# Performance work log

Hardware: AMD Instinct MI355X
Metric: run time of the kernel (lower is better)

The kernel has to match this reference:

```python
import jax, jax.numpy as jnp
import numpy as np

B_, S, I, H = 16, 2048, 256, 512


def setup_inputs() -> dict:
    key = jax.random.key(0)
    k0, k1, k2, k3, k4 = jax.random.split(key, 5)
    x = jax.random.normal(k0, (B_, S, I), dtype=jnp.float32)
    # stable LRU parameterization: lambda = exp(-exp(nu) + i*theta), |lambda| < 1
    nu = jax.random.uniform(k1, (H,), dtype=jnp.float32, minval=-3.0, maxval=0.0)
    theta = jax.random.uniform(k2, (H,), dtype=jnp.float32, minval=0.0, maxval=2.0 * np.pi)
    scale = np.float32(1.0 / np.sqrt(2 * I))
    B_re = jax.random.normal(k3, (H, I), dtype=jnp.float32) * scale
    B_im = jax.random.normal(k4, (H, I), dtype=jnp.float32) * scale
    return {"x": x, "nu": nu, "theta": theta, "B_re": B_re, "B_im": B_im}


def reference(x, nu, theta, B_re, B_im):
    # complex diagonal recurrence matrix, shape [H]
    lam = jnp.exp(-jnp.exp(nu) + 1j * theta).astype(jnp.complex64)
    # complex input projection Bx_t = (B_re + i B_im) @ x_t, shape [batch, seq, H]
    Bx = (jnp.einsum('bsi,hi->bsh', x, B_re)
          + 1j * jnp.einsum('bsi,hi->bsh', x, B_im)).astype(jnp.complex64)
    Bx_t = jnp.swapaxes(Bx, 0, 1)  # [seq, batch, H] for scan over time
    h0 = jnp.zeros((x.shape[0], lam.shape[0]), dtype=jnp.complex64)

    def step(h, bx):
        h = lam * h + bx  # h_t = lambda * h_{t-1} + B x_t
        return h, h

    _, outs = jax.lax.scan(step, h0, Bx_t)  # [seq, batch, H] complex
    outs = jnp.swapaxes(outs, 0, 1)  # [batch, seq, H]
    # concat_real_imag: [batch, seq, 2H] float32
    return jnp.concatenate([outs.real, outs.imag], axis=-1)
```

## Files before the change

### kernel.cpp

```cpp
#include <hip/hip_runtime.h>
#include <cstdint>
#include <cstddef>

#define BB 16
#define SS 2048
#define II 256
#define HH 512
#define MM (BB * SS)
#define NNC 1024
#define CHUNK 64
#define NCHUNK (SS / CHUNK)

using bf16x8 = __attribute__((ext_vector_type(8))) short;
using short8 = __attribute__((ext_vector_type(8))) short;
using f32x4  = __attribute__((ext_vector_type(4))) float;

typedef __attribute__((address_space(3))) uint32_t       lds_u32;
typedef __attribute__((address_space(1))) const uint32_t glb_u32;

__device__ __forceinline__ short f2bf(float f) {
    uint32_t u = __float_as_uint(f);
    u += 0x7fffu + ((u >> 16) & 1u);
    return (short)(u >> 16);
}
__device__ __forceinline__ uint32_t packf16(float a, float b) {
    union { _Float16 h[2]; uint32_t u; } cv;
    cv.h[0] = (_Float16)a; cv.h[1] = (_Float16)b;
    return cv.u;
}
__device__ __forceinline__ float2 unpackf16(uint32_t u) {
    union { uint32_t u; _Float16 h[2]; } cv; cv.u = u;
    return make_float2((float)cv.h[0], (float)cv.h[1]);
}

__global__ __launch_bounds__(256) void cvt_xb(const float4* __restrict__ x,
                                              short8* __restrict__ xb,
                                              const float* __restrict__ Bre,
                                              const float* __restrict__ Bim,
                                              short* __restrict__ Bc) {
    const int bid = blockIdx.x;
    if (bid < 4096) {
        int i = bid * 256 + threadIdx.x;
        float4 v0 = x[2 * i], v1 = x[2 * i + 1];
        short8 o;
        o[0]=f2bf(v0.x); o[1]=f2bf(v0.y); o[2]=f2bf(v0.z); o[3]=f2bf(v0.w);
        o[4]=f2bf(v1.x); o[5]=f2bf(v1.y); o[6]=f2bf(v1.z); o[7]=f2bf(v1.w);
        xb[i] = o;
    } else {
        int idx = (bid - 4096) * 256 + threadIdx.x;
        int row = idx >> 5;
        int k0  = (idx & 31) << 3;
        const float* src = ((row & 1) ? Bim : Bre) + (size_t)(row >> 1) * II + k0;
        float4 v0 = *(const float4*)src;
        float4 v1 = *(const float4*)(src + 4);
        short8 o;
        o[0]=f2bf(v0.x); o[1]=f2bf(v0.y); o[2]=f2bf(v0.z); o[3]=f2bf(v0.w);
        o[4]=f2bf(v1.x); o[5]=f2bf(v1.y); o[6]=f2bf(v1.z); o[7]=f2bf(v1.w);
        *(short8*)(Bc + (size_t)row * II + k0) = o;
    }
}

__global__ __launch_bounds__(256, 3) void gemm_pack(const short* __restrict__ Xb,
                                                    const short* __restrict__ Bc,
                                                    uint32_t* __restrict__ Y) {
    __shared__ short Al[2][128 * 32];
    __shared__ short Bl[2][128 * 32];

    const int xcd = blockIdx.x & 7;
    const int k   = blockIdx.x >> 3;
    const int mt  = xcd * 32 + (k >> 3);
    const int nt  = k & 7;
    const int m0 = mt * 128, n0 = nt * 128;
    const int t  = threadIdx.x;
    const int w  = t >> 6, l = t & 63;
    const int fr = l & 15, fg = l >> 4;
    const int wr = w >> 1, wc = w & 1;

    f32x4 acc[4][4] = {};

#pragma unroll
    for (int i = 0; i < 2; ++i) {
        const int ch = i * 256 + t;
        __builtin_amdgcn_global_load_lds(
            (glb_u32*)(Xb + (size_t)(m0 + (ch >> 2)) * II + ((ch & 3) << 3)),
            (lds_u32*)&Al[0][ch * 8], 16, 0, 0);
        __builtin_amdgcn_global_load_lds(
            (glb_u32*)(Bc + (size_t)(n0 + (ch >> 2)) * II + ((ch & 3) << 3)),
            (lds_u32*)&Bl[0][ch * 8], 16, 0, 0);
    }
    __syncthreads();

    for (int ks = 0; ks < 8; ++ks) {
        const int cur = ks & 1, nxt = cur ^ 1;
        if (ks < 7) {
#pragma unroll
            for (int i = 0; i < 2; ++i) {
                const int ch = i * 256 + t;
                __builtin_amdgcn_global_load_lds(
                    (glb_u32*)(Xb + (size_t)(m0 + (ch >> 2)) * II + (ks + 1) * 32 + ((ch & 3) << 3)),
                    (lds_u32*)&Al[nxt][ch * 8], 16, 0, 0);
                __builtin_amdgcn_global_load_lds(
                    (glb_u32*)(Bc + (size_t)(n0 + (ch >> 2)) * II + (ks + 1) * 32 + ((ch & 3) << 3)),
                    (lds_u32*)&Bl[nxt][ch * 8], 16, 0, 0);
            }
        }
        bf16x8 a[4], b[4];
#pragma unroll
        for (int mi = 0; mi < 4; ++mi)
            a[mi] = *(const bf16x8*)&Al[cur][(wr * 64 + mi * 16 + fr) * 32 + fg * 8];
#pragma unroll
        for (int ni = 0; ni < 4; ++ni)
            b[ni] = *(const bf16x8*)&Bl[cur][(wc * 64 + ni * 16 + fr) * 32 + fg * 8];
#pragma unroll
        for (int mi = 0; mi < 4; ++mi)
#pragma unroll
            for (int ni = 0; ni < 4; ++ni)
                acc[mi][ni] = __builtin_amdgcn_mfma_f32_16x16x32_bf16(
                    a[mi], b[ni], acc[mi][ni], 0, 0, 0);
        __syncthreads();
    }

#pragma unroll
    for (int mi = 0; mi < 4; ++mi)
#pragma unroll
        for (int ni = 0; ni < 4; ++ni) {
            const int row0 = m0 + wr * 64 + mi * 16 + fg * 4;
            const int ncol = n0 + wc * 64 + ni * 16 + fr;
#pragma unroll
            for (int r = 0; r < 4; ++r) {
                float v = acc[mi][ni][r];
                float o = __shfl_xor(v, 1);
                if (!(fr & 1))
                    Y[(size_t)(row0 + r) * HH + (ncol >> 1)] = packf16(v, o);
            }
        }
}

__global__ __launch_bounds__(512) void scan_e(const uint32_t* __restrict__ Y,
                                              const float* __restrict__ nu,
                                              const float* __restrict__ th,
                                              float2* __restrict__ E) {
    const int g = blockIdx.x;
    const int b = g >> 5, c = g & 31;
    const int h = threadIdx.x;
    const float env = __expf(nu[h]);
    const float rad = __expf(-env);
    float s, cs; __sincosf(th[h], &s, &cs);
    const float lre = rad * cs, lim = rad * s;
    const uint32_t* base = Y + ((size_t)b * SS + (size_t)c * CHUNK) * HH + h;
    float hre = 0.f, him = 0.f;
#pragma unroll 8
    for (int t = 0; t < CHUNK; ++t) {
        float2 y = unpackf16(base[(size_t)t * HH]);
        const float nr = lre * hre - lim * him + y.x;
        him = lre * him + lim * hre + y.y;
        hre = nr;
    }
    E[(size_t)g * HH + h] = make_float2(hre, him);
}

__global__ __launch_bounds__(512) void scan_final(const uint32_t* __restrict__ Y,
                                                  const float2* __restrict__ E,
                                                  const float* __restrict__ nu,
                                                  const float* __restrict__ th,
                                                  float* __restrict__ out) {
    const int g = blockIdx.x;
    const int b = g >> 5, c = g & 31;
    const int h = threadIdx.x;
    const float env = __expf(nu[h]);
    const float rad = __expf(-env);
    float s, cs; __sincosf(th[h], &s, &cs);
    const float lre = rad * cs, lim = rad * s;

    const float rL = __expf(-(float)CHUNK * env);
    float sL, cL; __sincosf((float)CHUNK * th[h], &sL, &cL);
    const float l64re = rL * cL, l64im = rL * sL;
    float pre = 0.f, pim = 0.f;
    for (int j = 0; j < c; ++j) {
        const float2 e = E[((size_t)(b * NCHUNK + j)) * HH + h];
        const float nr = l64re * pre - l64im * pim + e.x;
        pim = l64re * pim + l64im * pre + e.y;
        pre = nr;
    }

    float hre = pre, him = pim;
    const uint32_t* yb = Y + ((size_t)b * SS + (size_t)c * CHUNK) * HH + h;
    float* ob = out + ((size_t)b * SS + (size_t)c * CHUNK) * NNC;
#pragma unroll 4
    for (int t = 0; t < CHUNK; ++t) {
        float2 y = unpackf16(yb[(size_t)t * HH]);
        const float nr = lre * hre - lim * him + y.x;
        him = lre * him + lim * hre + y.y;
        hre = nr;
        ob[(size_t)t * NNC + h]      = hre;
        ob[(size_t)t * NNC + HH + h] = him;
    }
}

extern "C" void kernel_launch(void* const* d_in, const int* in_sizes, int n_in,
                              void* d_out, int out_size, void* d_ws, size_t ws_size,
                              hipStream_t stream) {
    const float* x   = (const float*)d_in[0];
    const float* nu  = (const float*)d_in[1];
    const float* th  = (const float*)d_in[2];
    const float* Bre = (const float*)d_in[3];
    const float* Bim = (const float*)d_in[4];
    float* out = (float*)d_out;

    char* ws = (char*)d_ws;
    short*    Xb = (short*)ws;
    short*    Bc = (short*)(ws + (size_t)MM * II * 2);
    uint32_t* Y  = (uint32_t*)(ws + (size_t)MM * II * 2 + (size_t)NNC * II * 2);
    float2*   E  = (float2*)((char*)Y + (size_t)MM * HH * 4);

    cvt_xb<<<4096 + 128, 256, 0, stream>>>((const float4*)x, (short8*)Xb, Bre, Bim, Bc);
    gemm_pack<<<(MM / 128) * (NNC / 128), 256, 0, stream>>>(Xb, Bc, Y);
    scan_e<<<BB * NCHUNK, HH, 0, stream>>>(Y, nu, th, E);
    scan_final<<<BB * NCHUNK, HH, 0, stream>>>(Y, E, nu, th, out);
}
```

Measured before the change: 90.61 us.

## Fuse x fp32-to-bf16 conversion into GEMM A-tile loading

Removes the separate pass that converted x to bf16 in a workspace buffer. The GEMM now reads fp32 x directly into registers, converts it, and writes it to a padded LDS tile (row stride 40), with the next tile's loads issued before the MFMAs. This drops a full write and re-read of the bf16 copy of x, but each GEMM block now reads fp32 x at twice the bytes, and x is re-read by all 8 N-tiles. It also adds VALU conversion work and register pressure inside the GEMM.

```diff
diff --git a/kernel.cpp b/kernel.cpp
--- a/kernel.cpp
+++ b/kernel.cpp
@@ -10,6 +10,7 @@
 #define NNC 1024
 #define CHUNK 64
 #define NCHUNK (SS / CHUNK)
+#define ALDW 40
 
 using bf16x8 = __attribute__((ext_vector_type(8))) short;
 using short8 = __attribute__((ext_vector_type(8))) short;
@@ -33,37 +34,25 @@
     return make_float2((float)cv.h[0], (float)cv.h[1]);
 }
 
-__global__ __launch_bounds__(256) void cvt_xb(const float4* __restrict__ x,
-                                              short8* __restrict__ xb,
-                                              const float* __restrict__ Bre,
-                                              const float* __restrict__ Bim,
-                                              short* __restrict__ Bc) {
-    const int bid = blockIdx.x;
-    if (bid < 4096) {
-        int i = bid * 256 + threadIdx.x;
-        float4 v0 = x[2 * i], v1 = x[2 * i + 1];
-        short8 o;
-        o[0]=f2bf(v0.x); o[1]=f2bf(v0.y); o[2]=f2bf(v0.z); o[3]=f2bf(v0.w);
-        o[4]=f2bf(v1.x); o[5]=f2bf(v1.y); o[6]=f2bf(v1.z); o[7]=f2bf(v1.w);
-        xb[i] = o;
-    } else {
-        int idx = (bid - 4096) * 256 + threadIdx.x;
-        int row = idx >> 5;
-        int k0  = (idx & 31) << 3;
-        const float* src = ((row & 1) ? Bim : Bre) + (size_t)(row >> 1) * II + k0;
-        float4 v0 = *(const float4*)src;
-        float4 v1 = *(const float4*)(src + 4);
-        short8 o;
-        o[0]=f2bf(v0.x); o[1]=f2bf(v0.y); o[2]=f2bf(v0.z); o[3]=f2bf(v0.w);
-        o[4]=f2bf(v1.x); o[5]=f2bf(v1.y); o[6]=f2bf(v1.z); o[7]=f2bf(v1.w);
-        *(short8*)(Bc + (size_t)row * II + k0) = o;
-    }
-}
-
-__global__ __launch_bounds__(256, 3) void gemm_pack(const short* __restrict__ Xb,
+__global__ __launch_bounds__(256) void cvt_b(const float* __restrict__ Bre,
+                                             const float* __restrict__ Bim,
+                                             short* __restrict__ Bc) {
+    int idx = blockIdx.x * 256 + threadIdx.x;
+    int row = idx >> 5;
+    int k0  = (idx & 31) << 3;
+    const float* src = ((row & 1) ? Bim : Bre) + (size_t)(row >> 1) * II + k0;
+    float4 v0 = *(const float4*)src;
+    float4 v1 = *(const float4*)(src + 4);
+    short8 o;
+    o[0]=f2bf(v0.x); o[1]=f2bf(v0.y); o[2]=f2bf(v0.z); o[3]=f2bf(v0.w);
+    o[4]=f2bf(v1.x); o[5]=f2bf(v1.y); o[6]=f2bf(v1.z); o[7]=f2bf(v1.w);
+    *(short8*)(Bc + (size_t)row * II + k0) = o;
+}
+
+__global__ __launch_bounds__(256, 3) void gemm_pack(const float* __restrict__ X,
                                                     const short* __restrict__ Bc,
                                                     uint32_t* __restrict__ Y) {
-    __shared__ short Al[2][128 * 32];
+    __shared__ short Al[2][128 * ALDW];
     __shared__ short Bl[2][128 * 32];
 
     const int xcd = blockIdx.x & 7;
@@ -76,15 +65,29 @@
     const int fr = l & 15, fg = l >> 4;
     const int wr = w >> 1, wc = w & 1;
 
+    const int arow = t >> 1, akh = t & 1;
+    const float* xrow = X + (size_t)(m0 + arow) * II + akh * 16;
+    short* aldst = &Al[0][arow * ALDW + akh * 16];
+
     f32x4 acc[4][4] = {};
 
+    {
+        float4 v0 = *(const float4*)(xrow + 0);
+        float4 v1 = *(const float4*)(xrow + 4);
+        float4 v2 = *(const float4*)(xrow + 8);
+        float4 v3 = *(const float4*)(xrow + 12);
+        short8 o0, o1;
+        o0[0]=f2bf(v0.x); o0[1]=f2bf(v0.y); o0[2]=f2bf(v0.z); o0[3]=f2bf(v0.w);
+        o0[4]=f2bf(v1.x); o0[5]=f2bf(v1.y); o0[6]=f2bf(v1.z); o0[7]=f2bf(v1.w);
+        o1[0]=f2bf(v2.x); o1[1]=f2bf(v2.y); o1[2]=f2bf(v2.z); o1[3]=f2bf(v2.w);
+        o1[4]=f2bf(v3.x); o1[5]=f2bf(v3.y); o1[6]=f2bf(v3.z); o1[7]=f2bf(v3.w);
+        *(short8*)(aldst + 0) = o0;
+        *(short8*)(aldst + 8) = o1;
+    }
 #pragma unroll
     for (int i = 0; i < 2; ++i) {
         const int ch = i * 256 + t;
         __builtin_amdgcn_global_load_lds(
-            (glb_u32*)(Xb + (size_t)(m0 + (ch >> 2)) * II + ((ch & 3) << 3)),
-            (lds_u32*)&Al[0][ch * 8], 16, 0, 0);
-        __builtin_amdgcn_global_load_lds(
             (glb_u32*)(Bc + (size_t)(n0 + (ch >> 2)) * II + ((ch & 3) << 3)),
             (lds_u32*)&Bl[0][ch * 8], 16, 0, 0);
     }
@@ -92,13 +95,16 @@
 
     for (int ks = 0; ks < 8; ++ks) {
         const int cur = ks & 1, nxt = cur ^ 1;
+        float4 v0, v1, v2, v3;
         if (ks < 7) {
+            const float* xs = xrow + (ks + 1) * 32;
+            v0 = *(const float4*)(xs + 0);
+            v1 = *(const float4*)(xs + 4);
+            v2 = *(const float4*)(xs + 8);
+            v3 = *(const float4*)(xs + 12);
 #pragma unroll
             for (int i = 0; i < 2; ++i) {
                 const int ch = i * 256 + t;
-                __builtin_amdgcn_global_load_lds(
-                    (glb_u32*)(Xb + (size_t)(m0 + (ch >> 2)) * II + (ks + 1) * 32 + ((ch & 3) << 3)),
-                    (lds_u32*)&Al[nxt][ch * 8], 16, 0, 0);
                 __builtin_amdgcn_global_load_lds(
                     (glb_u32*)(Bc + (size_t)(n0 + (ch >> 2)) * II + (ks + 1) * 32 + ((ch & 3) << 3)),
                     (lds_u32*)&Bl[nxt][ch * 8], 16, 0, 0);
@@ -107,7 +113,7 @@
         bf16x8 a[4], b[4];
 #pragma unroll
         for (int mi = 0; mi < 4; ++mi)
-            a[mi] = *(const bf16x8*)&Al[cur][(wr * 64 + mi * 16 + fr) * 32 + fg * 8];
+            a[mi] = *(const bf16x8*)&Al[cur][(wr * 64 + mi * 16 + fr) * ALDW + fg * 8];
 #pragma unroll
         for (int ni = 0; ni < 4; ++ni)
             b[ni] = *(const bf16x8*)&Bl[cur][(wc * 64 + ni * 16 + fr) * 32 + fg * 8];
@@ -117,6 +123,16 @@
             for (int ni = 0; ni < 4; ++ni)
                 acc[mi][ni] = __builtin_amdgcn_mfma_f32_16x16x32_bf16(
                     a[mi], b[ni], acc[mi][ni], 0, 0, 0);
+        if (ks < 7) {
+            short8 o0, o1;
+            o0[0]=f2bf(v0.x); o0[1]=f2bf(v0.y); o0[2]=f2bf(v0.z); o0[3]=f2bf(v0.w);
+            o0[4]=f2bf(v1.x); o0[5]=f2bf(v1.y); o0[6]=f2bf(v1.z); o0[7]=f2bf(v1.w);
+            o1[0]=f2bf(v2.x); o1[1]=f2bf(v2.y); o1[2]=f2bf(v2.z); o1[3]=f2bf(v2.w);
+            o1[4]=f2bf(v3.x); o1[5]=f2bf(v3.y); o1[6]=f2bf(v3.z); o1[7]=f2bf(v3.w);
+            short* ad = aldst + nxt * 128 * ALDW;
+            *(short8*)(ad + 0) = o0;
+            *(short8*)(ad + 8) = o1;
+        }
         __syncthreads();
     }
 
@@ -208,13 +224,12 @@
     float* out = (float*)d_out;
 
     char* ws = (char*)d_ws;
-    short*    Xb = (short*)ws;
-    short*    Bc = (short*)(ws + (size_t)MM * II * 2);
-    uint32_t* Y  = (uint32_t*)(ws + (size_t)MM * II * 2 + (size_t)NNC * II * 2);
+    short*    Bc = (short*)ws;
+    uint32_t* Y  = (uint32_t*)(ws + (size_t)NNC * II * 2);
     float2*   E  = (float2*)((char*)Y + (size_t)MM * HH * 4);
 
-    cvt_xb<<<4096 + 128, 256, 0, stream>>>((const float4*)x, (short8*)Xb, Bre, Bim, Bc);
-    gemm_pack<<<(MM / 128) * (NNC / 128), 256, 0, stream>>>(Xb, Bc, Y);
+    cvt_b<<<(NNC * II / 8) / 256, 256, 0, stream>>>(Bre, Bim, Bc);
+    gemm_pack<<<(MM / 128) * (NNC / 128), 256, 0, stream>>>(x, Bc, Y);
     scan_e<<<BB * NCHUNK, HH, 0, stream>>>(Y, nu, th, E);
     scan_final<<<BB * NCHUNK, HH, 0, stream>>>(Y, E, nu, th, out);
 }
```

Measured after the change: 94.17 us. 1.04x slower.
